# Kernel optimization log

Measured on AMD Instinct MI355X. Metric: run time of the kernel, lower is better.

## Reference

```python
import jax, jax.numpy as jnp
import numpy as np

N, K, DIM = 65536, 32, 64


def setup_inputs() -> dict:
    key = jax.random.key(0)
    k1, k2, k3, k4 = jax.random.split(key, 4)
    x = jax.random.normal(k1, (N, DIM), jnp.float32)
    log_pi = jax.random.normal(k2, (K, 1), jnp.float32)
    mu = jax.random.normal(k3, (K, DIM), jnp.float32)
    log_sigma_ = jax.random.normal(k4, (K, DIM, DIM), jnp.float32) / 100.0
    return {"x": x, "log_pi": log_pi, "mu": mu, "log_sigma_": log_sigma_}


def reference(x, log_pi, mu, log_sigma_):
    k, d = mu.shape
    # Faithful to torch: softmax over the size-1 last axis of (K,1) -> all ones.
    pi = jax.nn.softmax(log_pi, axis=-1)  # (K, 1)
    # scale_tril construction: strict lower triangle kept, diagonal -> exp(diag) + 1e-3
    diag = jnp.exp(jnp.diagonal(log_sigma_, axis1=-2, axis2=-1)) + 1e-3  # (K, d)
    L = jnp.tril(log_sigma_, -1) + jnp.eye(d, dtype=x.dtype) * diag[:, None, :]  # (K, d, d)
    # batched MVN log_prob via triangular solve
    diff = x[:, None, :] - mu[None, :, :]            # (N, K, d)
    b = jnp.transpose(diff, (1, 2, 0))               # (K, d, N)
    z = jax.scipy.linalg.solve_triangular(L, b, lower=True)  # (K, d, N)
    maha = jnp.sum(z * z, axis=1)                    # (K, N)
    logdet = jnp.sum(jnp.log(diag), axis=-1)         # (K,)
    logp = -0.5 * (maha + d * jnp.log(2.0 * jnp.pi)) - logdet[:, None]  # (K, N)
    p = jnp.exp(logp).T                              # (N, K)
    return jnp.log(jnp.matmul(p, pi).squeeze())      # (N,)
```

## Files before the change

kernel.cpp:

```cpp
#include <hip/hip_runtime.h>

#define KK 32
#define DD 64
#define NB 65536
#define PAD 68
#define FRAGS 12
#define SLOT (FRAGS * 64)
#define MREF 103.0f

typedef __attribute__((ext_vector_type(8))) short bf16x8;
typedef __attribute__((ext_vector_type(4))) float f32x4;

__device__ inline short f2bf(float f) {
  uint32_t u = __builtin_bit_cast(uint32_t, f);
  uint32_t r = (u + 0x7fffu + ((u >> 16) & 1u)) >> 16;
  return (short)(r & 0xffffu);
}
__device__ inline float bf2f(short h) {
  uint32_t u = ((uint32_t)(unsigned short)h) << 16;
  return __builtin_bit_cast(float, u);
}
__device__ inline uint4 pack8(const short* v) {
  uint4 u;
  u.x = (uint32_t)(unsigned short)v[0] | ((uint32_t)(unsigned short)v[1] << 16);
  u.y = (uint32_t)(unsigned short)v[2] | ((uint32_t)(unsigned short)v[3] << 16);
  u.z = (uint32_t)(unsigned short)v[4] | ((uint32_t)(unsigned short)v[5] << 16);
  u.w = (uint32_t)(unsigned short)v[6] | ((uint32_t)(unsigned short)v[7] << 16);
  return u;
}

__global__ __launch_bounds__(256) void md_prep(const float* __restrict__ ls,
                                               const float* __restrict__ mu,
                                               uint4* __restrict__ Bp,
                                               short* __restrict__ Whp,
                                               short* __restrict__ Wlp,
                                               float* __restrict__ Kc2) {
  __shared__ float Ls[DD * DD];
  __shared__ float Ys[DD * PAD];
  __shared__ float invdL[DD];
  __shared__ float muL[DD];
  __shared__ float cL[DD];
  const int k = blockIdx.x, t = threadIdx.x;
  const int j = t >> 2, sub = t & 3;
  const float* __restrict__ lsk = ls + (size_t)k * DD * DD;

#pragma unroll
  for (int it = 0; it < 4; ++it) {
    const int o = (it * 256 + t) * 4;
    *(float4*)&Ls[o] = *(const float4*)&lsk[o];
  }
  if (t < DD) muL[t] = mu[k * DD + t];
  __syncthreads();
  if (t < DD) invdL[t] = 1.0f / (expf(Ls[t * DD + t]) + 1e-3f);
  __syncthreads();

  const float invdj = invdL[j];
  float z[16];
#pragma unroll
  for (int mi = 0; mi < 16; ++mi) z[mi] = 0.f;
#pragma unroll
  for (int i = 0; i < DD; ++i) {
    float p = 0.f;
#pragma unroll
    for (int mi = 0; mi < 16; ++mi) {
      if (4 * mi < i) {
        const int m = 4 * mi + sub;
        p = fmaf(Ls[i * DD + m], (m < i) ? z[mi] : 0.f, p);
      }
    }
    p += __shfl_xor(p, 1, 64);
    p += __shfl_xor(p, 2, 64);
    const float zi = (i == j) ? invdj : -p * invdL[i];
    if (sub == (i & 3)) z[i >> 2] = zi;
  }
#pragma unroll
  for (int mi = 0; mi < 16; ++mi) Ys[(4 * mi + sub) * PAD + j] = z[mi];
  __syncthreads();

  {
    float p = 0.f;
#pragma unroll
    for (int mi = 0; mi < 16; ++mi) {
      const int m = 4 * mi + sub;
      p = fmaf(Ys[j * PAD + m], muL[m], p);
    }
    p += __shfl_xor(p, 1, 64);
    p += __shfl_xor(p, 2, 64);
    if (sub == 0) cL[j] = p;
  }
  __syncthreads();

  {
    float p = 0.f;
#pragma unroll
    for (int ii = 0; ii < 16; ++ii) {
      const int i = 4 * ii + sub;
      p = fmaf(Ys[i * PAD + j], cL[i], p);
    }
    p += __shfl_xor(p, 1, 64);
    p += __shfl_xor(p, 2, 64);
    if (sub == 0) {
      const short h = f2bf(p);
      Whp[k * DD + j] = h;
      Wlp[k * DD + j] = f2bf(p - bf2f(h));
    }
  }

  if (t < DD) {
    float r = -logf(invdL[t]) + 0.5f * cL[t] * cL[t];
#pragma unroll
    for (int off = 32; off > 0; off >>= 1) r += __shfl_down(r, off, 64);
    if (t == 0) Kc2[k] = MREF - 0.5f * (64.0f * 1.83787706640934534f) - r;
  }

  if (t < DD) {
    const int colp = t & 15, qp = t >> 4;
    uint4* slot = Bp + (size_t)k * SLOT;
#pragma unroll
    for (int s = 0; s < 2; ++s) {
#pragma unroll
      for (int ct = 0; ct < 4; ++ct) {
        if (s == 1 && ct < 2) continue;
        const int i = colp + 16 * ct;
        const float4 v0 = *(const float4*)&Ys[i * PAD + s * 32 + qp * 8];
        const float4 v1 = *(const float4*)&Ys[i * PAD + s * 32 + qp * 8 + 4];
        const float f[8] = {v0.x, v0.y, v0.z, v0.w, v1.x, v1.y, v1.z, v1.w};
        short hh[8], ll[8];
#pragma unroll
        for (int jj = 0; jj < 8; ++jj) {
          const short h = f2bf(f[jj]);
          hh[jj] = h;
          ll[jj] = f2bf(f[jj] - bf2f(h));
        }
        const int fi = 2 * ct + (s ? 4 : 0);
        slot[(fi + 0) * 64 + t] = pack8(hh);
        slot[(fi + 1) * 64 + t] = pack8(ll);
      }
    }
  }
}

__global__ __launch_bounds__(256, 2) void md_main(const float* __restrict__ x,
                                                  const uint4* __restrict__ Bp,
                                                  const short* __restrict__ Whp,
                                                  const short* __restrict__ Wlp,
                                                  const float* __restrict__ Kc2,
                                                  float* __restrict__ P) {
  const int tid = threadIdx.x, lane = tid & 63, w = tid >> 6;
  const int quarter = blockIdx.x & 3;
  const int sblk = blockIdx.x >> 2;
  const int base = sblk * 256 + w * 64;
  const int k0 = quarter * 8;
  const int col = lane & 15, q = lane >> 4;

  bf16x8 Xh[4][2], Xl[4][2];
#pragma unroll
  for (int Bt = 0; Bt < 4; ++Bt) {
#pragma unroll
    for (int s = 0; s < 2; ++s) {
      const float* src = x + (size_t)(base + Bt * 16 + col) * DD + s * 32 + q * 8;
      const float4 v0 = *(const float4*)src;
      const float4 v1 = *(const float4*)(src + 4);
      const float f[8] = {v0.x, v0.y, v0.z, v0.w, v1.x, v1.y, v1.z, v1.w};
      bf16x8 h, l;
#pragma unroll
      for (int jj = 0; jj < 8; ++jj) {
        const short hb = f2bf(f[jj]);
        h[jj] = hb;
        l[jj] = f2bf(f[jj] - bf2f(hb));
      }
      Xh[Bt][s] = h;
      Xl[Bt][s] = l;
    }
  }

  f32x4 crossD[4];
  {
    bf16x8 WhF[2], WlF[2];
    const int rr = col & 7;
#pragma unroll
    for (int s = 0; s < 2; ++s) {
      const size_t off = (size_t)(k0 + rr) * DD + s * 32 + q * 8;
      uint4 hv = *(const uint4*)(Whp + off);
      uint4 lv = *(const uint4*)(Wlp + off);
      if (col >= 8) { hv = (uint4){0, 0, 0, 0}; lv = (uint4){0, 0, 0, 0}; }
      WhF[s] = __builtin_bit_cast(bf16x8, hv);
      WlF[s] = __builtin_bit_cast(bf16x8, lv);
    }
#pragma unroll
    for (int Bt = 0; Bt < 4; ++Bt) {
      f32x4 zc = (f32x4){0.f, 0.f, 0.f, 0.f};
      zc = __builtin_amdgcn_mfma_f32_16x16x32_bf16(WhF[0], Xh[Bt][0], zc, 0, 0, 0);
      zc = __builtin_amdgcn_mfma_f32_16x16x32_bf16(WlF[0], Xh[Bt][0], zc, 0, 0, 0);
      zc = __builtin_amdgcn_mfma_f32_16x16x32_bf16(WhF[0], Xl[Bt][0], zc, 0, 0, 0);
      zc = __builtin_amdgcn_mfma_f32_16x16x32_bf16(WhF[1], Xh[Bt][1], zc, 0, 0, 0);
      zc = __builtin_amdgcn_mfma_f32_16x16x32_bf16(WlF[1], Xh[Bt][1], zc, 0, 0, 0);
      zc = __builtin_amdgcn_mfma_f32_16x16x32_bf16(WhF[1], Xl[Bt][1], zc, 0, 0, 0);
      crossD[Bt] = zc;
    }
  }

  const uint4* __restrict__ Bl = Bp + (size_t)k0 * SLOT + lane;

  uint4 F0[FRAGS], F1[FRAGS];
#pragma unroll
  for (int fi = 0; fi < FRAGS; ++fi) F0[fi] = Bl[fi * 64];

  float run_s[4] = {0.f, 0.f, 0.f, 0.f};

#pragma unroll
  for (int kk = 0; kk < 8; ++kk) {
    const int k = k0 + kk;
    const uint4* cur = (kk & 1) ? F1 : F0;
    uint4* nxt = (kk & 1) ? F0 : F1;
    if (kk < 7) {
      const uint4* __restrict__ src = Bl + (size_t)(kk + 1) * SLOT;
#pragma unroll
      for (int fi = 0; fi < FRAGS; ++fi) nxt[fi] = src[fi * 64];
    }
    const float kc = Kc2[k];

    f32x4 mah[4];
#pragma unroll
    for (int Bt = 0; Bt < 4; ++Bt) mah[Bt] = (f32x4){0.f, 0.f, 0.f, 0.f};

#pragma unroll
    for (int ct = 0; ct < 4; ++ct) {
      const bf16x8 A0h = __builtin_bit_cast(bf16x8, cur[2 * ct + 0]);
      const bf16x8 A0l = __builtin_bit_cast(bf16x8, cur[2 * ct + 1]);
      bf16x8 A1h{}, A1l{};
      if (ct >= 2) {
        A1h = __builtin_bit_cast(bf16x8, cur[2 * ct + 4]);
        A1l = __builtin_bit_cast(bf16x8, cur[2 * ct + 5]);
      }
#pragma unroll
      for (int Bt = 0; Bt < 4; ++Bt) {
        f32x4 z1 = (f32x4){0.f, 0.f, 0.f, 0.f};
        z1 = __builtin_amdgcn_mfma_f32_16x16x32_bf16(A0h, Xh[Bt][0], z1, 0, 0, 0);
        z1 = __builtin_amdgcn_mfma_f32_16x16x32_bf16(A0l, Xh[Bt][0], z1, 0, 0, 0);
        z1 = __builtin_amdgcn_mfma_f32_16x16x32_bf16(A0h, Xl[Bt][0], z1, 0, 0, 0);
        if (ct >= 2) {
          f32x4 z2 = (f32x4){0.f, 0.f, 0.f, 0.f};
          z2 = __builtin_amdgcn_mfma_f32_16x16x32_bf16(A1h, Xh[Bt][1], z2, 0, 0, 0);
          z2 = __builtin_amdgcn_mfma_f32_16x16x32_bf16(A1l, Xh[Bt][1], z2, 0, 0, 0);
          z2 = __builtin_amdgcn_mfma_f32_16x16x32_bf16(A1h, Xl[Bt][1], z2, 0, 0, 0);
          z1 += z2;
        }
        mah[Bt] += z1 * z1;
      }
    }

#pragma unroll
    for (int Bt = 0; Bt < 4; ++Bt) {
      float s = (mah[Bt][0] + mah[Bt][1]) + (mah[Bt][2] + mah[Bt][3]);
      s += __shfl_xor(s, 16, 64);
      s += __shfl_xor(s, 32, 64);
      const float cv = __shfl(crossD[Bt][kk & 3], (kk >> 2) * 16 + col, 64);
      const float tt = fmaf(-0.5f, s, kc + cv);
      run_s[Bt] += __expf(tt);
    }
  }

  if (q == 0) {
#pragma unroll
    for (int Bt = 0; Bt < 4; ++Bt) {
      const int sid = base + Bt * 16 + col;
      P[quarter * NB + sid] = run_s[Bt];
    }
  }
}

__global__ __launch_bounds__(256) void md_comb(const float* __restrict__ P,
                                               float* __restrict__ out) {
  const int n = blockIdx.x * 256 + threadIdx.x;
  const float S = (P[n] + P[NB + n]) + (P[2 * NB + n] + P[3 * NB + n]);
  out[n] = logf(S) - MREF;
}

extern "C" void kernel_launch(void* const* d_in, const int* in_sizes, int n_in,
                              void* d_out, int out_size, void* d_ws, size_t ws_size,
                              hipStream_t stream) {
  const float* x  = (const float*)d_in[0];
  const float* mu = (const float*)d_in[2];
  const float* ls = (const float*)d_in[3];
  float* out = (float*)d_out;

  char* ws = (char*)d_ws;
  uint4* Bp  = (uint4*)ws;
  float* P   = (float*)(ws + (size_t)KK * SLOT * 16);
  short* Whp = (short*)(P + 4 * NB);
  short* Wlp = Whp + KK * DD;
  float* Kc2 = (float*)(Wlp + KK * DD);

  md_prep<<<KK, 256, 0, stream>>>(ls, mu, Bp, Whp, Wlp, Kc2);
  md_main<<<1024, 256, 0, stream>>>(x, Bp, Whp, Wlp, Kc2, P);
  md_comb<<<NB / 256, 256, 0, stream>>>(P, out);
}
```

Measured before the change: 119.3 us.

## Stage factor tiles in LDS via direct global loads and fold mean into accumulator

The per-component inverse-factor fragments are now double-buffered in shared memory using global_load_lds, where before each wave loaded them into registers. This should cut register pressure and redundant global traffic across the four waves. The mean term is also handled differently: the MFMA accumulator is seeded with -L^{-1}mu instead of computing a separate cross term, which removes the extra MFMA pass, the shuffle and the prep-stage W/c^2 computation. In exchange it adds a block barrier per component iteration and LDS reads for every fragment.

```diff
diff --git a/kernel.cpp b/kernel.cpp
--- a/kernel.cpp
+++ b/kernel.cpp
@@ -29,17 +29,21 @@
   return u;
 }
 
+__device__ __forceinline__ void gl_lds16(const uint4* g, uint4* l) {
+  __builtin_amdgcn_global_load_lds(
+      (__attribute__((address_space(1))) void*)g,
+      (__attribute__((address_space(3))) void*)l, 16, 0, 0);
+}
+
 __global__ __launch_bounds__(256) void md_prep(const float* __restrict__ ls,
                                                const float* __restrict__ mu,
                                                uint4* __restrict__ Bp,
-                                               short* __restrict__ Whp,
-                                               short* __restrict__ Wlp,
+                                               float* __restrict__ Cc,
                                                float* __restrict__ Kc2) {
   __shared__ float Ls[DD * DD];
   __shared__ float Ys[DD * PAD];
   __shared__ float invdL[DD];
   __shared__ float muL[DD];
-  __shared__ float cL[DD];
   const int k = blockIdx.x, t = threadIdx.x;
   const int j = t >> 2, sub = t & 3;
   const float* __restrict__ lsk = ls + (size_t)k * DD * DD;
@@ -86,28 +90,11 @@
     }
     p += __shfl_xor(p, 1, 64);
     p += __shfl_xor(p, 2, 64);
-    if (sub == 0) cL[j] = p;
-  }
-  __syncthreads();
-
-  {
-    float p = 0.f;
-#pragma unroll
-    for (int ii = 0; ii < 16; ++ii) {
-      const int i = 4 * ii + sub;
-      p = fmaf(Ys[i * PAD + j], cL[i], p);
-    }
-    p += __shfl_xor(p, 1, 64);
-    p += __shfl_xor(p, 2, 64);
-    if (sub == 0) {
-      const short h = f2bf(p);
-      Whp[k * DD + j] = h;
-      Wlp[k * DD + j] = f2bf(p - bf2f(h));
-    }
+    if (sub == 0) Cc[k * DD + j] = p;
   }
 
   if (t < DD) {
-    float r = -logf(invdL[t]) + 0.5f * cL[t] * cL[t];
+    float r = -logf(invdL[t]);
 #pragma unroll
     for (int off = 32; off > 0; off >>= 1) r += __shfl_down(r, off, 64);
     if (t == 0) Kc2[k] = MREF - 0.5f * (64.0f * 1.83787706640934534f) - r;
@@ -142,10 +129,10 @@
 
 __global__ __launch_bounds__(256, 2) void md_main(const float* __restrict__ x,
                                                   const uint4* __restrict__ Bp,
-                                                  const short* __restrict__ Whp,
-                                                  const short* __restrict__ Wlp,
+                                                  const float* __restrict__ Cc,
                                                   const float* __restrict__ Kc2,
                                                   float* __restrict__ P) {
+  __shared__ uint4 lds4[2 * SLOT];
   const int tid = threadIdx.x, lane = tid & 63, w = tid >> 6;
   const int quarter = blockIdx.x & 3;
   const int sblk = blockIdx.x >> 2;
@@ -174,68 +161,47 @@
     }
   }
 
-  f32x4 crossD[4];
   {
-    bf16x8 WhF[2], WlF[2];
-    const int rr = col & 7;
-#pragma unroll
-    for (int s = 0; s < 2; ++s) {
-      const size_t off = (size_t)(k0 + rr) * DD + s * 32 + q * 8;
-      uint4 hv = *(const uint4*)(Whp + off);
-      uint4 lv = *(const uint4*)(Wlp + off);
-      if (col >= 8) { hv = (uint4){0, 0, 0, 0}; lv = (uint4){0, 0, 0, 0}; }
-      WhF[s] = __builtin_bit_cast(bf16x8, hv);
-      WlF[s] = __builtin_bit_cast(bf16x8, lv);
-    }
-#pragma unroll
-    for (int Bt = 0; Bt < 4; ++Bt) {
-      f32x4 zc = (f32x4){0.f, 0.f, 0.f, 0.f};
-      zc = __builtin_amdgcn_mfma_f32_16x16x32_bf16(WhF[0], Xh[Bt][0], zc, 0, 0, 0);
-      zc = __builtin_amdgcn_mfma_f32_16x16x32_bf16(WlF[0], Xh[Bt][0], zc, 0, 0, 0);
-      zc = __builtin_amdgcn_mfma_f32_16x16x32_bf16(WhF[0], Xl[Bt][0], zc, 0, 0, 0);
-      zc = __builtin_amdgcn_mfma_f32_16x16x32_bf16(WhF[1], Xh[Bt][1], zc, 0, 0, 0);
-      zc = __builtin_amdgcn_mfma_f32_16x16x32_bf16(WlF[1], Xh[Bt][1], zc, 0, 0, 0);
-      zc = __builtin_amdgcn_mfma_f32_16x16x32_bf16(WhF[1], Xl[Bt][1], zc, 0, 0, 0);
-      crossD[Bt] = zc;
-    }
-  }
-
-  const uint4* __restrict__ Bl = Bp + (size_t)k0 * SLOT + lane;
-
-  uint4 F0[FRAGS], F1[FRAGS];
-#pragma unroll
-  for (int fi = 0; fi < FRAGS; ++fi) F0[fi] = Bl[fi * 64];
+    const uint4* src = Bp + (size_t)k0 * SLOT;
+#pragma unroll
+    for (int it = 0; it < 3; ++it)
+      gl_lds16(src + it * 256 + w * 64 + lane, &lds4[it * 256 + w * 64]);
+  }
+  __syncthreads();
 
   float run_s[4] = {0.f, 0.f, 0.f, 0.f};
 
 #pragma unroll
   for (int kk = 0; kk < 8; ++kk) {
     const int k = k0 + kk;
-    const uint4* cur = (kk & 1) ? F1 : F0;
-    uint4* nxt = (kk & 1) ? F0 : F1;
+    const int p = kk & 1;
     if (kk < 7) {
-      const uint4* __restrict__ src = Bl + (size_t)(kk + 1) * SLOT;
-#pragma unroll
-      for (int fi = 0; fi < FRAGS; ++fi) nxt[fi] = src[fi * 64];
+      const uint4* src = Bp + (size_t)(k + 1) * SLOT;
+#pragma unroll
+      for (int it = 0; it < 3; ++it)
+        gl_lds16(src + it * 256 + w * 64 + lane,
+                 &lds4[(1 - p) * SLOT + it * 256 + w * 64]);
     }
     const float kc = Kc2[k];
 
+    const uint4* buf = &lds4[p * SLOT];
     f32x4 mah[4];
 #pragma unroll
     for (int Bt = 0; Bt < 4; ++Bt) mah[Bt] = (f32x4){0.f, 0.f, 0.f, 0.f};
 
 #pragma unroll
     for (int ct = 0; ct < 4; ++ct) {
-      const bf16x8 A0h = __builtin_bit_cast(bf16x8, cur[2 * ct + 0]);
-      const bf16x8 A0l = __builtin_bit_cast(bf16x8, cur[2 * ct + 1]);
+      const bf16x8 A0h = *(const bf16x8*)&buf[(2 * ct + 0) * 64 + lane];
+      const bf16x8 A0l = *(const bf16x8*)&buf[(2 * ct + 1) * 64 + lane];
       bf16x8 A1h{}, A1l{};
       if (ct >= 2) {
-        A1h = __builtin_bit_cast(bf16x8, cur[2 * ct + 4]);
-        A1l = __builtin_bit_cast(bf16x8, cur[2 * ct + 5]);
-      }
+        A1h = *(const bf16x8*)&buf[(2 * ct + 4) * 64 + lane];
+        A1l = *(const bf16x8*)&buf[(2 * ct + 5) * 64 + lane];
+      }
+      const f32x4 ci = -*(const f32x4*)&Cc[k * DD + ct * 16 + q * 4];
 #pragma unroll
       for (int Bt = 0; Bt < 4; ++Bt) {
-        f32x4 z1 = (f32x4){0.f, 0.f, 0.f, 0.f};
+        f32x4 z1 = ci;
         z1 = __builtin_amdgcn_mfma_f32_16x16x32_bf16(A0h, Xh[Bt][0], z1, 0, 0, 0);
         z1 = __builtin_amdgcn_mfma_f32_16x16x32_bf16(A0l, Xh[Bt][0], z1, 0, 0, 0);
         z1 = __builtin_amdgcn_mfma_f32_16x16x32_bf16(A0h, Xl[Bt][0], z1, 0, 0, 0);
@@ -255,10 +221,11 @@
       float s = (mah[Bt][0] + mah[Bt][1]) + (mah[Bt][2] + mah[Bt][3]);
       s += __shfl_xor(s, 16, 64);
       s += __shfl_xor(s, 32, 64);
-      const float cv = __shfl(crossD[Bt][kk & 3], (kk >> 2) * 16 + col, 64);
-      const float tt = fmaf(-0.5f, s, kc + cv);
+      const float tt = fmaf(-0.5f, s, kc);
       run_s[Bt] += __expf(tt);
     }
+
+    if (kk < 7) __syncthreads();
   }
 
   if (q == 0) {
@@ -288,11 +255,10 @@
   char* ws = (char*)d_ws;
   uint4* Bp  = (uint4*)ws;
   float* P   = (float*)(ws + (size_t)KK * SLOT * 16);
-  short* Whp = (short*)(P + 4 * NB);
-  short* Wlp = Whp + KK * DD;
-  float* Kc2 = (float*)(Wlp + KK * DD);
-
-  md_prep<<<KK, 256, 0, stream>>>(ls, mu, Bp, Whp, Wlp, Kc2);
-  md_main<<<1024, 256, 0, stream>>>(x, Bp, Whp, Wlp, Kc2, P);
+  float* Cc  = P + 4 * NB;
+  float* Kc2 = Cc + KK * DD;
+
+  md_prep<<<KK, 256, 0, stream>>>(ls, mu, Bp, Cc, Kc2);
+  md_main<<<1024, 256, 0, stream>>>(x, Bp, Cc, Kc2, P);
   md_comb<<<NB / 256, 256, 0, stream>>>(P, out);
 }
```

Measured after the change: 118.7 us. No clear change (-0.6%).
